# Kernel optimization log

Measured on AMD Instinct MI355X. Metric: run time of the kernel, lower is better.

## Reference

```python
import jax, jax.numpy as jnp
import numpy as np

IN_C, OUT_C, K, STRIDE, PAD = 128, 256, 3, 1, 1

def setup_inputs() -> dict:
    key = jax.random.key(0)
    kx, kw = jax.random.split(key)
    x = jax.random.normal(kx, (32, IN_C, 56, 56), dtype=jnp.float32)
    # xavier_uniform_ on W: bound = sqrt(6 / (fan_in + fan_out)), fan = C*K*K
    fan_in = IN_C * K * K
    fan_out = OUT_C * K * K
    bound = float(np.sqrt(6.0 / (fan_in + fan_out)))
    W = jax.random.uniform(kw, (OUT_C, IN_C, K, K), dtype=jnp.float32, minval=-bound, maxval=bound)
    b = jnp.zeros((OUT_C,), dtype=jnp.float32)
    return {"x": x, "W": W, "b": b}

def reference(x, W, b):
    # Direct conv: NCHW input, OIHW weights -> NCHW output
    out = jax.lax.conv_general_dilated(
        x, W,
        window_strides=(STRIDE, STRIDE),
        padding=[(PAD, PAD), (PAD, PAD)],
        dimension_numbers=("NCHW", "OIHW", "NCHW"),
    )
    return out + b[None, :, None, None]
```

## Files before the change

### kernel.cpp

```cpp
#include <hip/hip_runtime.h>


typedef unsigned short u16;
typedef _Float16 f16x8 __attribute__((ext_vector_type(8)));
typedef float f32x4 __attribute__((ext_vector_type(4)));

#define CIN    128
#define COUT   256
#define HW     56
#define NPIX   3136
#define TOTPIX 100352
#define NKT    18

#define WAITVM2 asm volatile("s_waitcnt vmcnt(2)" ::: "memory")
#define WAITVM0 asm volatile("s_waitcnt vmcnt(0)" ::: "memory")
#define BARRIER asm volatile("s_barrier" ::: "memory")

__device__ __forceinline__ void gload16(const void* g, void* l) {
  __builtin_amdgcn_global_load_lds(
      (const __attribute__((address_space(1))) void*)g,
      (__attribute__((address_space(3))) void*)l, 16, 0, 0);
}

__device__ __forceinline__ u16 f2h(float f) {
  _Float16 h = (_Float16)f;
  return __builtin_bit_cast(u16, h);
}

__global__ void prep_w(const float* __restrict__ W, u16* __restrict__ Wt,
                       u16* __restrict__ zp) {
  int e = blockIdx.x * 256 + threadIdx.x;
  if (blockIdx.x == 0 && threadIdx.x < 128) zp[threadIdx.x] = 0;
  int j    = e & 7;
  int ocl  = (e >> 3) & 127;
  int k8   = (e >> 10) & 7;
  int half = (e >> 13) & 1;
  int t    = e >> 14;
  int oc = half * 128 + ocl;
  int ic = (t & 1) * 64 + k8 * 8 + j;
  Wt[e] = f2h(W[(oc * CIN + ic) * 9 + (t >> 1)]);
}

__global__ void prep_x(const float* __restrict__ x, u16* __restrict__ xt) {
  __shared__ unsigned int tile[64 * 65];
  int b = blockIdx.x;
  int n = b / 49;
  int hw0 = (b % 49) * 64;
  int tid = threadIdx.x;
  const float* xb = x + (size_t)n * CIN * NPIX + hw0;
  #pragma unroll
  for (int i = 0; i < 16; ++i) {
    int e = tid + i * 256;
    int icp = e >> 6;
    int pix = e & 63;
    float a = xb[(size_t)(2 * icp) * NPIX + pix];
    float c = xb[(size_t)(2 * icp + 1) * NPIX + pix];
    tile[pix * 65 + icp] = (unsigned)f2h(a) | ((unsigned)f2h(c) << 16);
  }
  __syncthreads();
  u16* outb = xt + (size_t)(n * NPIX + hw0) * CIN;
  #pragma unroll
  for (int i = 0; i < 4; ++i) {
    int e = tid + i * 256;
    int pix = e >> 4;
    int q = e & 15;
    uint4 v;
    v.x = tile[pix * 65 + q * 4 + 0];
    v.y = tile[pix * 65 + q * 4 + 1];
    v.z = tile[pix * 65 + q * 4 + 2];
    v.w = tile[pix * 65 + q * 4 + 3];
    *(uint4*)(outb + (size_t)pix * CIN + q * 8) = v;
  }
}

#define QUAD(MH, NH)                                                          \
  do {                                                                        \
    __builtin_amdgcn_s_setprio(1);                                            \
    _Pragma("unroll") for (int mq = 0; mq < 4; ++mq)                          \
    _Pragma("unroll") for (int nf = 0; nf < 2; ++nf)                          \
    _Pragma("unroll") for (int kk = 0; kk < 2; ++kk)                          \
      acc[(MH)*4 + mq][(NH)*2 + nf] =                                         \
          __builtin_amdgcn_mfma_f32_16x16x32_f16(                             \
              af[mq][kk], bf[(NH)][nf][kk], acc[(MH)*4 + mq][(NH)*2 + nf],    \
              0, 0, 0);                                                       \
    __builtin_amdgcn_s_setprio(0);                                            \
  } while (0)

#define READB(BUFO, NH)                                                       \
  do {                                                                        \
    _Pragma("unroll") for (int nf = 0; nf < 2; ++nf)                          \
    _Pragma("unroll") for (int kk = 0; kk < 2; ++kk)                          \
      bf[(NH)][nf][kk] = *(const f16x8*)&lds[(BUFO) + 16384 + bhalf * 8192 +  \
          ((kk * 4 + lg) * 128 + bpl + (NH)*32 + nf * 16) * 8];               \
  } while (0)

__global__ __launch_bounds__(512, 2) void conv_mfma(
    const u16* __restrict__ Wt, const u16* __restrict__ xt,
    const float* __restrict__ bias, float* __restrict__ out,
    const u16* __restrict__ zp) {
  __shared__ __align__(16) u16 lds[65536];

  int tid  = threadIdx.x;
  int lane = tid & 63;
  int wv   = tid >> 6;
  int bid  = blockIdx.x;
  int ptile = (bid & 7) * 49 + (bid >> 3);

  int wm = wv >> 2, wn = wv & 3;
  int l15 = lane & 15, lg = lane >> 4;
  int bhalf = wn >> 1;
  int bpl = (wn & 1) * 64 + l15;

  int pixl = tid & 127, tph = tid >> 7;
  int p0 = ptile * 256 + pixl, p1 = p0 + 128;
  int n0 = p0 / NPIX, r0 = p0 % NPIX, y0 = r0 / HW, x0 = r0 % HW;
  int n1 = p1 / NPIX, r1 = p1 % NPIX, y1 = r1 / HW, x1 = r1 % HW;
  const char* xb0 = (const char*)xt + ((size_t)n0 * NPIX + r0) * 256;
  const char* xb1 = (const char*)xt + ((size_t)n1 * NPIX + r1) * 256;
  const char* wsrc = (const char*)Wt + tid * 16;
  const char* zpc = (const char*)zp;

  auto stageA = [&](int tn, int h) {
    const char* src = wsrc + (size_t)(tn * 2048 + h * 1024) * 16;
    u16* dst = &lds[(tn & 1) * 32768 + h * 8192 + tid * 8];
    gload16(src, dst);
    gload16(src + 8192, dst + 4096);
  };
  auto stageB = [&](int tn, int h, const char* src) {
    u16* dst = &lds[(tn & 1) * 32768 + 16384 + h * 8192 + tid * 8];
    gload16(src, dst);
    gload16(src + 64, dst + 4096);
  };
  auto bsrc = [&](int tap, int icb, int h) -> const char* {
    int t3 = tap / 3;
    int dh = t3 - 1, dw = (tap - t3 * 3) - 1;
    int ih = (h ? y1 : y0) + dh, iw = (h ? x1 : x0) + dw;
    const char* xb = h ? xb1 : xb0;
    return ((unsigned)ih < HW && (unsigned)iw < HW)
        ? xb + (dh * HW + dw) * 256 + icb * 128 + tph * 16
        : zpc + tph * 16;
  };

  f32x4 acc[8][4] = {};
  f16x8 af[4][2], bf[2][2][2];

  auto readA = [&](int bufo, int mh) {
    #pragma unroll
    for (int mq = 0; mq < 4; ++mq)
      #pragma unroll
      for (int kk = 0; kk < 2; ++kk)
        af[mq][kk] = *(const f16x8*)&lds[bufo + wm * 8192 +
            ((kk * 4 + lg) * 128 + mh * 64 + mq * 16 + l15) * 8];
  };

  stageA(0, 0); stageB(0, 0, bsrc(0, 0, 0));
  stageA(0, 1); stageB(0, 1, bsrc(0, 0, 1));

  for (int t = 0; t < NKT; ++t) {
    int bufo = (t & 1) * 32768;
    int tn = t + 1;
    const char *sb0 = zpc, *sb1 = zpc;
    if (tn < NKT) { sb0 = bsrc(tn >> 1, tn & 1, 0); sb1 = bsrc(tn >> 1, tn & 1, 1); }
    if (tn < NKT) { stageA(tn, 0); WAITVM2; } else { WAITVM0; }
    BARRIER;
    readA(bufo, 0); READB(bufo, 0);
    QUAD(0, 0);
    BARRIER;
    READB(bufo, 1);
    if (tn < NKT) stageB(tn, 0, sb0);
    BARRIER;
    QUAD(0, 1);
    BARRIER;
    readA(bufo, 1);
    if (tn < NKT) stageA(tn, 1);
    BARRIER;
    QUAD(1, 1);
    BARRIER;
    if (tn < NKT) stageB(tn, 1, sb1);
    BARRIER;
    QUAD(1, 0);
    BARRIER;
  }

  #pragma unroll
  for (int nf4 = 0; nf4 < 4; ++nf4) {
    int p = ptile * 256 + wn * 64 + nf4 * 16 + l15;
    int n = p / NPIX, hw = p % NPIX;
    float* ob = out + (size_t)n * COUT * NPIX + hw;
    #pragma unroll
    for (int mi = 0; mi < 8; ++mi) {
      int oc = wm * 128 + mi * 16 + lg * 4;
      f32x4 bv = *(const f32x4*)&bias[oc];
      #pragma unroll
      for (int r = 0; r < 4; ++r)
        ob[(size_t)(oc + r) * NPIX] = acc[mi][nf4][r] + bv[r];
    }
  }
}

__global__ void conv_naive(const float* __restrict__ x, const float* __restrict__ W,
                           const float* __restrict__ b, float* __restrict__ out) {
  int idx = blockIdx.x * 256 + threadIdx.x;
  int hw = idx % NPIX;
  int tmp = idx / NPIX;
  int oc = tmp % COUT;
  int n = tmp / COUT;
  int h = hw / HW, w = hw % HW;
  float acc = b[oc];
  for (int ic = 0; ic < CIN; ++ic) {
    const float* xr = x + (size_t)(n * CIN + ic) * NPIX;
    const float* wr = W + (size_t)(oc * CIN + ic) * 9;
    #pragma unroll
    for (int kh = 0; kh < 3; ++kh) {
      int ih = h + kh - 1;
      if ((unsigned)ih >= HW) continue;
      #pragma unroll
      for (int kw = 0; kw < 3; ++kw) {
        int iw = w + kw - 1;
        if ((unsigned)iw >= HW) continue;
        acc += xr[ih * HW + iw] * wr[kh * 3 + kw];
      }
    }
  }
  out[idx] = acc;
}

extern "C" void kernel_launch(void* const* d_in, const int* in_sizes, int n_in,
                              void* d_out, int out_size, void* d_ws, size_t ws_size,
                              hipStream_t stream) {
  const float* x = (const float*)d_in[0];
  const float* W = (const float*)d_in[1];
  const float* b = (const float*)d_in[2];
  float* out = (float*)d_out;

  const size_t ZP_OFF = 0;
  const size_t WT_OFF = 256;
  const size_t XT_OFF = 256 + 589824;
  const size_t NEED = XT_OFF + (size_t)TOTPIX * CIN * 2;

  if (ws_size < NEED) {
    conv_naive<<<TOTPIX * COUT / 256, 256, 0, stream>>>(x, W, b, out);
    return;
  }
  char* ws = (char*)d_ws;
  u16* zp = (u16*)(ws + ZP_OFF);
  u16* Wt = (u16*)(ws + WT_OFF);
  u16* xt = (u16*)(ws + XT_OFF);

  prep_w<<<1152, 256, 0, stream>>>(W, Wt, zp);
  prep_x<<<1568, 256, 0, stream>>>(x, xt);
  conv_mfma<<<392, 512, 0, stream>>>(Wt, xt, b, out, zp);
}
```

Baseline: 101.7 us.

## Store fp16 input as channel-group-major NC8HW8 to coalesce B-tile loads

Changes the transposed activation layout from NHWC to [n][ic/8][hw][8], so the 16-byte-per-lane loads in the conv kernel's B staging walk contiguous pixels within one channel group rather than striding 256 bytes per pixel. The prep_x writes and the conv address math are updated to match, with the second load offset by four channel groups. The epilogue loop order is also swapped so that consecutive stores hit the same output row across pixel fragments. The intent is better coalescing on the activation reads and writes, at the cost of slightly more address arithmetic per staged load.

Measured after the change: 96.16 us. -5.5%, faster.

```diff
diff --git a/kernel.cpp b/kernel.cpp
--- a/kernel.cpp
+++ b/kernel.cpp
@@ -58,18 +58,17 @@
     tile[pix * 65 + icp] = (unsigned)f2h(a) | ((unsigned)f2h(c) << 16);
   }
   __syncthreads();
-  u16* outb = xt + (size_t)(n * NPIX + hw0) * CIN;
   #pragma unroll
   for (int i = 0; i < 4; ++i) {
     int e = tid + i * 256;
-    int pix = e >> 4;
-    int q = e & 15;
+    int g = e >> 6;
+    int pix = e & 63;
     uint4 v;
-    v.x = tile[pix * 65 + q * 4 + 0];
-    v.y = tile[pix * 65 + q * 4 + 1];
-    v.z = tile[pix * 65 + q * 4 + 2];
-    v.w = tile[pix * 65 + q * 4 + 3];
-    *(uint4*)(outb + (size_t)pix * CIN + q * 8) = v;
+    v.x = tile[pix * 65 + g * 4 + 0];
+    v.y = tile[pix * 65 + g * 4 + 1];
+    v.z = tile[pix * 65 + g * 4 + 2];
+    v.w = tile[pix * 65 + g * 4 + 3];
+    *(uint4*)(xt + ((size_t)(n * 16 + g) * NPIX + hw0 + pix) * 8) = v;
   }
 }
 
@@ -115,8 +114,7 @@
   int p0 = ptile * 256 + pixl, p1 = p0 + 128;
   int n0 = p0 / NPIX, r0 = p0 % NPIX, y0 = r0 / HW, x0 = r0 % HW;
   int n1 = p1 / NPIX, r1 = p1 % NPIX, y1 = r1 / HW, x1 = r1 % HW;
-  const char* xb0 = (const char*)xt + ((size_t)n0 * NPIX + r0) * 256;
-  const char* xb1 = (const char*)xt + ((size_t)n1 * NPIX + r1) * 256;
+  const char* xtb = (const char*)xt;
   const char* wsrc = (const char*)Wt + tid * 16;
   const char* zpc = (const char*)zp;
 
@@ -126,19 +124,19 @@
     gload16(src, dst);
     gload16(src + 8192, dst + 4096);
   };
+  auto bsrc = [&](int tap, int ich, int h) -> const char* {
+    int t3 = tap / 3;
+    int dh = t3 - 1, dw = (tap - t3 * 3) - 1;
+    int y = (h ? y1 : y0) + dh, xx = (h ? x1 : x0) + dw;
+    if ((unsigned)y >= HW || (unsigned)xx >= HW) return zpc;
+    int n = h ? n1 : n0;
+    int rsh = (h ? r1 : r0) + dh * HW + dw;
+    return xtb + ((size_t)(n * 16 + ich * 8 + tph) * NPIX + rsh) * 16;
+  };
   auto stageB = [&](int tn, int h, const char* src) {
     u16* dst = &lds[(tn & 1) * 32768 + 16384 + h * 8192 + tid * 8];
     gload16(src, dst);
-    gload16(src + 64, dst + 4096);
-  };
-  auto bsrc = [&](int tap, int icb, int h) -> const char* {
-    int t3 = tap / 3;
-    int dh = t3 - 1, dw = (tap - t3 * 3) - 1;
-    int ih = (h ? y1 : y0) + dh, iw = (h ? x1 : x0) + dw;
-    const char* xb = h ? xb1 : xb0;
-    return ((unsigned)ih < HW && (unsigned)iw < HW)
-        ? xb + (dh * HW + dw) * 256 + icb * 128 + tph * 16
-        : zpc + tph * 16;
+    gload16(src == zpc ? zpc : src + (size_t)4 * NPIX * 16, dst + 4096);
   };
 
   f32x4 acc[8][4] = {};
@@ -182,18 +180,23 @@
     BARRIER;
   }
 
+  float* ob[4];
   #pragma unroll
   for (int nf4 = 0; nf4 < 4; ++nf4) {
     int p = ptile * 256 + wn * 64 + nf4 * 16 + l15;
     int n = p / NPIX, hw = p % NPIX;
-    float* ob = out + (size_t)n * COUT * NPIX + hw;
+    ob[nf4] = out + (size_t)n * COUT * NPIX + hw;
+  }
+  #pragma unroll
+  for (int mi = 0; mi < 8; ++mi) {
+    int oc = wm * 128 + mi * 16 + lg * 4;
+    f32x4 bv = *(const f32x4*)&bias[oc];
     #pragma unroll
-    for (int mi = 0; mi < 8; ++mi) {
-      int oc = wm * 128 + mi * 16 + lg * 4;
-      f32x4 bv = *(const f32x4*)&bias[oc];
+    for (int r = 0; r < 4; ++r) {
+      size_t row = (size_t)(oc + r) * NPIX;
       #pragma unroll
-      for (int r = 0; r < 4; ++r)
-        ob[(size_t)(oc + r) * NPIX] = acc[mi][nf4][r] + bv[r];
+      for (int nf4 = 0; nf4 < 4; ++nf4)
+        ob[nf4][row] = acc[mi][nf4][r] + bv[r];
     }
   }
 }
```
